# Performance work log

Measured on AMD Instinct MI355X. Metric: run time of the kernel, lower is better.

## Reference

```python
import math
import jax, jax.numpy as jnp
import numpy as np

B, S, D, H = 2, 2048, 1024, 16
DH = D // H
EPS = 1e-5


def setup_inputs() -> dict:
    key = jax.random.key(0)
    ks = jax.random.split(key, 8)
    def lin(k, din, dout):
        return jax.random.normal(k, (din, dout), dtype=jnp.float32) / math.sqrt(din)
    return {
        "x": jax.random.normal(ks[0], (B, S, D), dtype=jnp.float32),
        "attention_mask": jnp.ones((B, S), dtype=jnp.int32),
        "Wq": lin(ks[1], D, D),
        "Wk": lin(ks[2], D, D),
        "Wv": lin(ks[3], D, D),
        "Wo": lin(ks[4], D, D),
        "W1": lin(ks[5], D, 4 * D),
        "W2": lin(ks[6], 2 * D, D),
        "gamma1": jnp.ones((D,), jnp.float32),
        "beta1": jnp.zeros((D,), jnp.float32),
        "gamma2": jnp.ones((D,), jnp.float32),
        "beta2": jnp.zeros((D,), jnp.float32),
    }


def layernorm(x, gamma, beta):
    mu = jnp.mean(x, axis=-1, keepdims=True)
    xc = x - mu
    var = jnp.mean(xc * xc, axis=-1, keepdims=True)
    return gamma * (xc / jnp.sqrt(var + EPS)) + beta


def softmax_last(x):
    x = x - jnp.max(x, axis=-1, keepdims=True)
    e = jnp.exp(x)
    return e / jnp.sum(e, axis=-1, keepdims=True)


def mhsa(x, attention_mask, Wq, Wk, Wv, Wo, causal=True):
    b, s, d = x.shape
    q = (x @ Wq).reshape(b, s, H, DH).transpose(0, 2, 1, 3)  # [b,h,s,dh]
    k = (x @ Wk).reshape(b, s, H, DH).transpose(0, 2, 1, 3)
    v = (x @ Wv).reshape(b, s, H, DH).transpose(0, 2, 1, 3)
    score = jnp.einsum("bhqd,bhkd->bhqk", q, k) / math.sqrt(DH)
    if causal:
        cmask = jnp.tril(jnp.ones((s, s), dtype=bool))
        score = jnp.where(cmask[None, None], score, -jnp.inf)
    key_mask = attention_mask.astype(bool)[:, None, None, :]  # [b,1,1,s]
    score = jnp.where(key_mask, score, -jnp.inf)
    attn = softmax_last(score)
    out = jnp.einsum("bhqk,bhkd->bhqd", attn, v)
    out = out.transpose(0, 2, 1, 3).reshape(b, s, d)
    return out @ Wo


def reference(x, attention_mask, Wq, Wk, Wv, Wo, W1, W2, gamma1, beta1, gamma2, beta2):
    x1 = x + mhsa(layernorm(x, gamma1, beta1), attention_mask, Wq, Wk, Wv, Wo, causal=True)
    h = layernorm(x1, gamma2, beta2) @ W1          # [b,s,4d]
    left, right = h[:, :, : 2 * D], h[:, :, 2 * D :]
    glu = left * jax.nn.sigmoid(right)             # [b,s,2d]
    return x1 + glu @ W2
```

## Files before the change

kernel.cpp:

```cpp
#include <hip/hip_runtime.h>
#include <hip/hip_bf16.h>
#include <math.h>

#define BB 2
#define SS 2048
#define DD 1024
#define HH 16
#define DH 64
#define NTOK (BB * SS)
#define LN_EPS 1e-5f
#define BIGNEG -1e30f

typedef __attribute__((ext_vector_type(8))) short bf16x8;
typedef __attribute__((ext_vector_type(4))) float f32x4;

static __device__ __forceinline__ unsigned short f2bu(float f) {
    __hip_bfloat16 h = __float2bfloat16(f);
    return *(unsigned short*)&h;
}

static __device__ __forceinline__ void async16(const void* g, void* l) {
    __builtin_amdgcn_global_load_lds((const __attribute__((address_space(1))) void*)g,
                                     (__attribute__((address_space(3))) void*)l, 16, 0, 0);
}


__global__ __launch_bounds__(256) void prep_kernel(const float* __restrict__ Wq,
                                                   const float* __restrict__ Wk,
                                                   const float* __restrict__ Wv,
                                                   const float* __restrict__ Wo,
                                                   const float* __restrict__ W1,
                                                   const float* __restrict__ W2,
                                                   __hip_bfloat16* __restrict__ wqkvt,
                                                   __hip_bfloat16* __restrict__ wot,
                                                   __hip_bfloat16* __restrict__ w1t,
                                                   __hip_bfloat16* __restrict__ w2t,
                                                   const float* __restrict__ x,
                                                   const float* __restrict__ gamma,
                                                   const float* __restrict__ beta,
                                                   __hip_bfloat16* __restrict__ lnb) {
    __shared__ float t[32][33];
    __shared__ float red[256];
    const int bid = blockIdx.x;
    const int tid = threadIdx.x;

    if (bid >= 10240) {
        const int row = bid - 10240;
        const float* xp = x + (size_t)row * DD;
        float vals[4];
        float s = 0.f;
#pragma unroll
        for (int i = 0; i < 4; ++i) {
            float v = xp[tid + i * 256];
            vals[i] = v;
            s += v;
        }
        red[tid] = s;
        __syncthreads();
        for (int st = 128; st > 0; st >>= 1) {
            if (tid < st) red[tid] += red[tid + st];
            __syncthreads();
        }
        const float mu = red[0] * (1.0f / DD);
        __syncthreads();
        float sq = 0.f;
#pragma unroll
        for (int i = 0; i < 4; ++i) {
            float d = vals[i] - mu;
            sq += d * d;
        }
        red[tid] = sq;
        __syncthreads();
        for (int st = 128; st > 0; st >>= 1) {
            if (tid < st) red[tid] += red[tid + st];
            __syncthreads();
        }
        const float rinv = rsqrtf(red[0] * (1.0f / DD) + LN_EPS);
        __hip_bfloat16* op = lnb + (size_t)row * DD;
#pragma unroll
        for (int i = 0; i < 4; ++i) {
            int j = tid + i * 256;
            op[j] = __float2bfloat16(gamma[j] * ((vals[i] - mu) * rinv) + beta[j]);
        }
        return;
    }

    const float* W;
    __hip_bfloat16* Wt;
    int K, N, tile;
    if (bid < 4096) {
        const int m = bid >> 10;
        tile = bid & 1023;
        W = (m == 0) ? Wq : (m == 1) ? Wk : (m == 2) ? Wv : Wo;
        Wt = (m < 3) ? (wqkvt + (size_t)m * 1024 * 1024) : wot;
        K = 1024; N = 1024;
    } else if (bid < 8192) {
        tile = bid - 4096; W = W1; Wt = w1t; K = 1024; N = 4096;
    } else {
        tile = bid - 8192; W = W2; Wt = w2t; K = 2048; N = 1024;
    }
    const int nt = N >> 5;
    const int n0 = (tile % nt) * 32, k0 = (tile / nt) * 32;
    const int tx = tid & 31, ty = tid >> 5;
#pragma unroll
    for (int i = 0; i < 4; ++i)
        t[ty + 8 * i][tx] = W[(size_t)(k0 + ty + 8 * i) * N + n0 + tx];
    __syncthreads();
#pragma unroll
    for (int i = 0; i < 4; ++i)
        Wt[(size_t)(n0 + ty + 8 * i) * K + k0 + tx] = __float2bfloat16(t[tx][ty + 8 * i]);
}

__global__ __launch_bounds__(256) void ln_kernel(const float* __restrict__ x,
                                                 const float* __restrict__ gamma,
                                                 const float* __restrict__ beta,
                                                 __hip_bfloat16* __restrict__ out) {
    const int row = blockIdx.x;
    const int tid = threadIdx.x;
    __shared__ float red[256];

    const float* xp = x + (size_t)row * DD;
    float vals[4];
    float s = 0.f;
#pragma unroll
    for (int i = 0; i < 4; ++i) {
        float v = xp[tid + i * 256];
        vals[i] = v;
        s += v;
    }
    red[tid] = s;
    __syncthreads();
    for (int st = 128; st > 0; st >>= 1) {
        if (tid < st) red[tid] += red[tid + st];
        __syncthreads();
    }
    const float mu = red[0] * (1.0f / DD);
    __syncthreads();
    float sq = 0.f;
#pragma unroll
    for (int i = 0; i < 4; ++i) {
        float d = vals[i] - mu;
        sq += d * d;
    }
    red[tid] = sq;
    __syncthreads();
    for (int st = 128; st > 0; st >>= 1) {
        if (tid < st) red[tid] += red[tid + st];
        __syncthreads();
    }
    const float rinv = rsqrtf(red[0] * (1.0f / DD) + LN_EPS);

    __hip_bfloat16* op = out + (size_t)row * DD;
#pragma unroll
    for (int i = 0; i < 4; ++i) {
        int j = tid + i * 256;
        op[j] = __float2bfloat16(gamma[j] * ((vals[i] - mu) * rinv) + beta[j]);
    }
}

__global__ __launch_bounds__(256) void vtrans(const __hip_bfloat16* __restrict__ qkvb_,
                                              __hip_bfloat16* __restrict__ VT_) {
    const unsigned short* src = (const unsigned short*)qkvb_;
    unsigned short* dst = (unsigned short*)VT_;
    __shared__ unsigned short t[64][65];
    const int c0 = (blockIdx.x & 15) << 6;
    const int t0 = (blockIdx.x >> 4) << 6;
    const int tx = threadIdx.x & 63, ty = threadIdx.x >> 6;
#pragma unroll
    for (int i = 0; i < 16; ++i)
        t[ty + 4 * i][tx] = src[(size_t)(t0 + ty + 4 * i) * 3072 + 2048 + c0 + tx];
    __syncthreads();
#pragma unroll
    for (int i = 0; i < 16; ++i)
        dst[(size_t)(c0 + ty + 4 * i) * 4096 + t0 + tx] = t[tx][ty + 4 * i];
}

template <int RES, int EPI>
__global__ __launch_bounds__(256) void mfma_gemm(const __hip_bfloat16* __restrict__ A,
                                                 const __hip_bfloat16* __restrict__ Bt,
                                                 const void* __restrict__ res,
                                                 void* __restrict__ out,
                                                 int M, int N, int K) {
    __shared__ short As[128 * 64];
    __shared__ short Bs[128 * 64];
    const int tid = threadIdx.x;
    const int lane = tid & 63;
    const int wave = tid >> 6;
    const int row0 = blockIdx.y * 128;
    const int col0 = blockIdx.x * 128;
    const int wr = (wave >> 1) * 64;
    const int wc = (wave & 1) * 64;
    const int l15 = lane & 15;
    const int quad = lane >> 4;
    const int s7 = l15 & 7;

    f32x4 acc[4][4] = {};

    for (int k0 = 0; k0 < K; k0 += 64) {
#pragma unroll
        for (int r = 0; r < 4; ++r) {
            const int ec = r * 256 + tid;
            const int ar = ec >> 3, d = ec & 7;
            const int ao = (d ^ (ar & 7)) << 3;
            async16(&A[(size_t)(row0 + ar) * K + k0 + ao], &As[ec << 3]);
            async16(&Bt[(size_t)(col0 + ar) * K + k0 + ao], &Bs[ec << 3]);
        }
        __syncthreads();
#pragma unroll
        for (int kk = 0; kk < 2; ++kk) {
            const int co = (((kk << 2) | quad) ^ s7) << 3;
            bf16x8 af[4], bfr[4];
#pragma unroll
            for (int i = 0; i < 4; ++i)
                af[i] = *(const bf16x8*)&As[(wr + i * 16 + l15) * 64 + co];
#pragma unroll
            for (int j = 0; j < 4; ++j)
                bfr[j] = *(const bf16x8*)&Bs[(wc + j * 16 + l15) * 64 + co];
#pragma unroll
            for (int i = 0; i < 4; ++i)
#pragma unroll
                for (int j = 0; j < 4; ++j)
                    acc[i][j] = __builtin_amdgcn_mfma_f32_16x16x32_bf16(af[i], bfr[j], acc[i][j], 0, 0, 0);
        }
        __syncthreads();
    }

    const int r4 = quad * 4;
#pragma unroll
    for (int i = 0; i < 4; ++i) {
#pragma unroll
        for (int j = 0; j < 4; ++j) {
            const int orow0 = row0 + wr + i * 16 + r4;
            const int ocol = col0 + wc + j * 16 + l15;
#pragma unroll
            for (int rg = 0; rg < 4; ++rg) {
                const size_t oi = (size_t)(orow0 + rg) * N + ocol;
                float v = acc[i][j][rg];
                if constexpr (RES == 1) v += ((const float*)res)[oi];
                if constexpr (EPI == 0) ((float*)out)[oi] = v;
                if constexpr (EPI == 1) ((__hip_bfloat16*)out)[oi] = __float2bfloat16(v);
            }
        }
    }
}

template <int RES, int EPI>
__global__ __launch_bounds__(256) void mfma_gemm_n64(const __hip_bfloat16* __restrict__ A,
                                                     const __hip_bfloat16* __restrict__ Bt,
                                                     const void* __restrict__ res,
                                                     void* __restrict__ out,
                                                     int N, int K, int colTiles) {
    __shared__ short As[128 * 64];
    __shared__ short Bs[64 * 64];
    const int tid = threadIdx.x;
    const int lane = tid & 63;
    const int wave = tid >> 6;
    const int cpx = gridDim.x >> 3;
    const int wg = (blockIdx.x & 7) * cpx + (blockIdx.x >> 3);
    const int row0 = (wg / colTiles) * 128;
    const int col0 = (wg % colTiles) * 64;
    const int wr = wave * 32;
    const int l15 = lane & 15;
    const int quad = lane >> 4;
    const int s7 = l15 & 7;

    f32x4 acc[2][4] = {};

    for (int k0 = 0; k0 < K; k0 += 64) {
#pragma unroll
        for (int r = 0; r < 4; ++r) {
            const int ec = r * 256 + tid;
            const int ar = ec >> 3, d = ec & 7;
            const int ao = (d ^ (ar & 7)) << 3;
            async16(&A[(size_t)(row0 + ar) * K + k0 + ao], &As[ec << 3]);
        }
#pragma unroll
        for (int r = 0; r < 2; ++r) {
            const int ec = r * 256 + tid;
            const int ar = ec >> 3, d = ec & 7;
            const int ao = (d ^ (ar & 7)) << 3;
            async16(&Bt[(size_t)(col0 + ar) * K + k0 + ao], &Bs[ec << 3]);
        }
        __syncthreads();
#pragma unroll
        for (int kk = 0; kk < 2; ++kk) {
            const int co = (((kk << 2) | quad) ^ s7) << 3;
            bf16x8 af[2], bfr[4];
#pragma unroll
            for (int i = 0; i < 2; ++i)
                af[i] = *(const bf16x8*)&As[(wr + i * 16 + l15) * 64 + co];
#pragma unroll
            for (int j = 0; j < 4; ++j)
                bfr[j] = *(const bf16x8*)&Bs[(j * 16 + l15) * 64 + co];
#pragma unroll
            for (int i = 0; i < 2; ++i)
#pragma unroll
                for (int j = 0; j < 4; ++j)
                    acc[i][j] = __builtin_amdgcn_mfma_f32_16x16x32_bf16(af[i], bfr[j], acc[i][j], 0, 0, 0);
        }
        __syncthreads();
    }

    const int r4 = quad * 4;
#pragma unroll
    for (int i = 0; i < 2; ++i) {
#pragma unroll
        for (int j = 0; j < 4; ++j) {
            const int orow0 = row0 + wr + i * 16 + r4;
            const int ocol = col0 + j * 16 + l15;
#pragma unroll
            for (int rg = 0; rg < 4; ++rg) {
                const size_t oi = (size_t)(orow0 + rg) * N + ocol;
                float v = acc[i][j][rg];
                if constexpr (RES == 1) v += ((const float*)res)[oi];
                if constexpr (EPI == 0) ((float*)out)[oi] = v;
                if constexpr (EPI == 1) ((__hip_bfloat16*)out)[oi] = __float2bfloat16(v);
            }
        }
    }
}

__global__ __launch_bounds__(256) void mfma_gemm_glu64(const __hip_bfloat16* __restrict__ A,
                                                       const __hip_bfloat16* __restrict__ Bt,
                                                       __hip_bfloat16* __restrict__ out) {
    __shared__ short As[128 * 64];
    __shared__ short Bl[64 * 64];
    __shared__ short Br[64 * 64];
    const int tid = threadIdx.x;
    const int lane = tid & 63;
    const int wave = tid >> 6;
    const int cpx = gridDim.x >> 3;
    const int wg = (blockIdx.x & 7) * cpx + (blockIdx.x >> 3);
    const int row0 = (wg >> 5) * 128;
    const int col0 = (wg & 31) * 64;
    const int wr = wave * 32;
    const int l15 = lane & 15;
    const int quad = lane >> 4;
    const int s7 = l15 & 7;

    f32x4 accl[2][4] = {};
    f32x4 accr[2][4] = {};

    for (int k0 = 0; k0 < 1024; k0 += 64) {
#pragma unroll
        for (int r = 0; r < 4; ++r) {
            const int ec = r * 256 + tid;
            const int ar = ec >> 3, d = ec & 7;
            const int ao = (d ^ (ar & 7)) << 3;
            async16(&A[(size_t)(row0 + ar) * 1024 + k0 + ao], &As[ec << 3]);
        }
#pragma unroll
        for (int r = 0; r < 2; ++r) {
            const int ec = r * 256 + tid;
            const int ar = ec >> 3, d = ec & 7;
            const int ao = (d ^ (ar & 7)) << 3;
            async16(&Bt[(size_t)(col0 + ar) * 1024 + k0 + ao], &Bl[ec << 3]);
            async16(&Bt[(size_t)(2048 + col0 + ar) * 1024 + k0 + ao], &Br[ec << 3]);
        }
        __syncthreads();
#pragma unroll
        for (int kk = 0; kk < 2; ++kk) {
            const int co = (((kk << 2) | quad) ^ s7) << 3;
            bf16x8 af[2], bl[4], br[4];
#pragma unroll
            for (int i = 0; i < 2; ++i)
                af[i] = *(const bf16x8*)&As[(wr + i * 16 + l15) * 64 + co];
#pragma unroll
            for (int j = 0; j < 4; ++j) {
                bl[j] = *(const bf16x8*)&Bl[(j * 16 + l15) * 64 + co];
                br[j] = *(const bf16x8*)&Br[(j * 16 + l15) * 64 + co];
            }
#pragma unroll
            for (int i = 0; i < 2; ++i)
#pragma unroll
                for (int j = 0; j < 4; ++j) {
                    accl[i][j] = __builtin_amdgcn_mfma_f32_16x16x32_bf16(af[i], bl[j], accl[i][j], 0, 0, 0);
                    accr[i][j] = __builtin_amdgcn_mfma_f32_16x16x32_bf16(af[i], br[j], accr[i][j], 0, 0, 0);
                }
        }
        __syncthreads();
    }

    const int r4 = quad * 4;
#pragma unroll
    for (int i = 0; i < 2; ++i) {
#pragma unroll
        for (int j = 0; j < 4; ++j) {
#pragma unroll
            for (int rg = 0; rg < 4; ++rg) {
                const int orow = row0 + wr + i * 16 + r4 + rg;
                const int ocol = col0 + j * 16 + l15;
                const float l = accl[i][j][rg];
                const float r = accr[i][j][rg];
                out[(size_t)orow * 2048 + ocol] =
                    __float2bfloat16(l * (1.f / (1.f + __expf(-r))));
            }
        }
    }
}

#define KADV (64 * 3072)
#define RESCALE_THR 8.f
__global__ __launch_bounds__(256, 4) void flash_mfma(const __hip_bfloat16* __restrict__ qkv_,
                                                     const __hip_bfloat16* __restrict__ VT_,
                                                     const int* __restrict__ mask,
                                                     __hip_bfloat16* __restrict__ attnb) {
    const unsigned short* qkv = (const unsigned short*)qkv_;
    const unsigned short* VT = (const unsigned short*)VT_;
    __shared__ __align__(16) short Ks[2][64 * 64];
    __shared__ __align__(16) short Vt[2][64 * 64];
    __shared__ __align__(16) short Ps[4][16 * 64];

    const int tid = threadIdx.x;
    const int lane = tid & 63;
    const int wave = tid >> 6;
    const int l15 = lane & 15;
    const int quad = lane >> 4;
    const int s7 = l15 & 7;

    const int xcd = blockIdx.x & 7;
    const int slot = blockIdx.x >> 3;
    const int bh = xcd + ((slot & 3) << 3);
    const int v = slot >> 2;
    const int vr = v & 7, vs = v >> 3;
    const int qt = (vs == 0) ? 31 - vr : (vs == 1) ? vr : (vs == 2) ? 23 - vr : 8 + vr;
    const int h = bh & 15;
    const int b = bh >> 4;
    const int q0 = qt * 64 + wave * 16;

    const int e0 = tid, e1 = 256 + tid;
    const int r0 = e0 >> 3, d0 = e0 & 7, r1 = e1 >> 3, d1 = e1 & 7;
    const unsigned short* kp0 = qkv + (size_t)(b * SS + r0) * 3072 + 1024 + h * 64 + ((d0 ^ (r0 & 7)) << 3);
    const unsigned short* kp1 = qkv + (size_t)(b * SS + r1) * 3072 + 1024 + h * 64 + ((d1 ^ (r1 & 7)) << 3);
    const unsigned short* vp0 = VT + (size_t)(h * 64 + r0) * 4096 + b * SS + ((d0 ^ (r0 & 7)) << 3);
    const unsigned short* vp1 = VT + (size_t)(h * 64 + r1) * 4096 + b * SS + ((d1 ^ (r1 & 7)) << 3);
    short* const kd0a = &Ks[0][e0 << 3]; short* const kd0b = &Ks[1][e0 << 3];
    short* const kd1a = &Ks[0][e1 << 3]; short* const kd1b = &Ks[1][e1 << 3];
    short* const vd0a = &Vt[0][e0 << 3]; short* const vd0b = &Vt[1][e0 << 3];
    short* const vd1a = &Vt[0][e1 << 3]; short* const vd1b = &Vt[1][e1 << 3];

    const int* const mrow = mask + b * SS;

    bf16x8 aq[2];
#pragma unroll
    for (int ks = 0; ks < 2; ++ks)
        aq[ks] = *(const bf16x8*)(qkv + (size_t)(b * SS + q0 + l15) * 3072 +
                                  h * 64 + ks * 32 + quad * 8);

    f32x4 O[4];
#pragma unroll
    for (int i = 0; i < 4; ++i) O[i] = (f32x4){0.f, 0.f, 0.f, 0.f};
    float m_r = BIGNEG, l_r = 0.f;

    const int nch = qt + 1;

    async16(kp0, kd0a); async16(kp1, kd1a);
    async16(vp0, vd0a); async16(vp1, vd1a);
    kp0 += KADV; kp1 += KADV; vp0 += 64; vp1 += 64;

    for (int c = 0; c < nch; ++c) {
        const int cur = c & 1;
        __syncthreads();

        if (c + 1 < nch) {
            async16(kp0, cur ? kd0a : kd0b);
            async16(kp1, cur ? kd1a : kd1b);
            async16(vp0, cur ? vd0a : vd0b);
            async16(vp1, cur ? vd1a : vd1b);
            kp0 += KADV; kp1 += KADV; vp0 += 64; vp1 += 64;
        }

        const int kb = c << 6;
        const int dq = q0 - kb;
        if (dq + 15 < 0) continue;

        int ktmax = ((dq + 15) >> 4) + 1;
        if (ktmax > 4) ktmax = 4;
        int ktfull = (dq - 15) >= 0 ? ((dq - 15) >> 4) + 1 : 0;
        if (ktfull > 4) ktfull = 4;
        const short* Kc = &Ks[cur][0];
        const short* Vc = &Vt[cur][0];

        int4 mv[4];
#pragma unroll
        for (int kt = 0; kt < 4; ++kt) {
            if (kt >= ktmax) break;
            mv[kt] = *(const int4*)&mrow[kb + kt * 16 + quad * 4];
        }

        f32x4 S[4];
        __builtin_amdgcn_s_setprio(1);
#pragma unroll
        for (int kt = 0; kt < 4; ++kt) {
            if (kt >= ktmax) break;
            const bf16x8 bk0 = *(const bf16x8*)&Kc[(kt * 16 + l15) * 64 + ((quad ^ s7) << 3)];
            const bf16x8 bk1 = *(const bf16x8*)&Kc[(kt * 16 + l15) * 64 + (((4 | quad) ^ s7) << 3)];
            f32x4 z = {0.f, 0.f, 0.f, 0.f};
            z = __builtin_amdgcn_mfma_f32_16x16x32_bf16(bk0, aq[0], z, 0, 0, 0);
            S[kt] = __builtin_amdgcn_mfma_f32_16x16x32_bf16(bk1, aq[1], z, 0, 0, 0);
        }
        __builtin_amdgcn_s_setprio(0);

        const int qrow = q0 + l15;
#pragma unroll
        for (int kt = 0; kt < 4; ++kt) {
            if (kt >= ktmax) break;
            const int* mm = (const int*)&mv[kt];
#pragma unroll
            for (int rg = 0; rg < 4; ++rg) {
                float s = fmaf(S[kt][rg], 0.125f, mm[rg] ? 0.f : BIGNEG);
                if (kt >= ktfull) {
                    const int key = kb + kt * 16 + quad * 4 + rg;
                    s = (key <= qrow) ? s : BIGNEG;
                }
                S[kt][rg] = s;
            }
        }

        float tmax = BIGNEG;
#pragma unroll
        for (int kt = 0; kt < 4; ++kt) {
            if (kt >= ktmax) break;
            tmax = fmaxf(tmax, fmaxf(fmaxf(S[kt][0], S[kt][1]),
                                     fmaxf(S[kt][2], S[kt][3])));
        }
        tmax = fmaxf(tmax, __shfl_xor(tmax, 16));
        tmax = fmaxf(tmax, __shfl_xor(tmax, 32));

        if (__any(tmax > m_r + RESCALE_THR)) {
            const float mn = fmaxf(m_r, tmax);
            const float alpha = __expf(m_r - mn);
            m_r = mn;
            l_r *= alpha;
#pragma unroll
            for (int nt = 0; nt < 4; ++nt)
#pragma unroll
                for (int rg = 0; rg < 4; ++rg)
                    O[nt][rg] *= alpha;
        }

        float rsum = 0.f;
#pragma unroll
        for (int kt = 0; kt < 4; ++kt) {
            if (kt >= ktmax) break;
#pragma unroll
            for (int rg = 0; rg < 4; ++rg)
                S[kt][rg] = __expf(S[kt][rg] - m_r);
            rsum += (S[kt][0] + S[kt][1]) + (S[kt][2] + S[kt][3]);
        }
        rsum += __shfl_xor(rsum, 16);
        rsum += __shfl_xor(rsum, 32);
        l_r += rsum;

        short* Pw = &Ps[wave][0];
        asm volatile("s_waitcnt lgkmcnt(0)" ::: "memory");
#pragma unroll
        for (int kt = 0; kt < 4; ++kt) {
            if (kt >= ktmax) break;
            const int ch = (kt << 1) | (quad >> 1);
            const int base = (l15 << 6) + (((ch ^ s7) << 3) | ((quad & 1) << 2));
            const unsigned p0 = ((unsigned)f2bu(S[kt][1]) << 16) | f2bu(S[kt][0]);
            const unsigned p1 = ((unsigned)f2bu(S[kt][3]) << 16) | f2bu(S[kt][2]);
            *(unsigned*)&Pw[base] = p0;
            *(unsigned*)&Pw[base + 2] = p1;
        }
        const int kkmax = (ktmax + 1) >> 1;
        if (ktmax & 1) {
            const int ch = (ktmax << 1) | (quad >> 1);
            const int base = (l15 << 6) + (((ch ^ s7) << 3) | ((quad & 1) << 2));
            *(unsigned*)&Pw[base] = 0;
            *(unsigned*)&Pw[base + 2] = 0;
        }
        asm volatile("s_waitcnt lgkmcnt(0)" ::: "memory");
        __builtin_amdgcn_s_setprio(1);
#pragma unroll
        for (int kk = 0; kk < 2; ++kk) {
            if (kk >= kkmax) break;
            const bf16x8 bp = *(const bf16x8*)&Pw[(l15 << 6) + ((((kk << 2) | quad) ^ s7) << 3)];
#pragma unroll
            for (int nt = 0; nt < 4; ++nt) {
                const bf16x8 av = *(const bf16x8*)&Vc[(nt * 16 + l15) * 64 +
                                                     ((((kk << 2) | quad) ^ s7) << 3)];
                O[nt] = __builtin_amdgcn_mfma_f32_16x16x32_bf16(av, bp, O[nt], 0, 0, 0);
            }
        }
        __builtin_amdgcn_s_setprio(0);
    }

    const float inv = 1.f / l_r;
    unsigned short* op = (unsigned short*)attnb +
                         (size_t)(b * SS + q0 + l15) * 1024 + h * 64 + quad * 4;
#pragma unroll
    for (int nt = 0; nt < 4; ++nt) {
        const float o0 = O[nt][0] * inv, o1 = O[nt][1] * inv;
        const float o2 = O[nt][2] * inv, o3 = O[nt][3] * inv;
        const unsigned long long pk =
            (unsigned long long)(((unsigned)f2bu(o3) << 16) | f2bu(o2)) << 32 |
            (((unsigned)f2bu(o1) << 16) | f2bu(o0));
        *(unsigned long long*)(op + nt * 16) = pk;
    }
}

extern "C" void kernel_launch(void* const* d_in, const int* in_sizes, int n_in,
                              void* d_out, int out_size, void* d_ws, size_t ws_size,
                              hipStream_t stream) {
    const float* x  = (const float*)d_in[0];
    const int* mask = (const int*)d_in[1];
    const float* Wq = (const float*)d_in[2];
    const float* Wk = (const float*)d_in[3];
    const float* Wv = (const float*)d_in[4];
    const float* Wo = (const float*)d_in[5];
    const float* W1 = (const float*)d_in[6];
    const float* W2 = (const float*)d_in[7];
    const float* g1 = (const float*)d_in[8];
    const float* b1 = (const float*)d_in[9];
    const float* g2 = (const float*)d_in[10];
    const float* b2 = (const float*)d_in[11];

    const size_t MB = 1024 * 1024;
    uint8_t* ws = (uint8_t*)d_ws;
    __hip_bfloat16* wqkvt = (__hip_bfloat16*)(ws);
    __hip_bfloat16* wot   = (__hip_bfloat16*)(ws + 6 * MB);
    __hip_bfloat16* w1t   = (__hip_bfloat16*)(ws + 8 * MB);
    __hip_bfloat16* w2t   = (__hip_bfloat16*)(ws + 16 * MB);
    __hip_bfloat16* lnb   = (__hip_bfloat16*)(ws + 20 * MB);
    __hip_bfloat16* qkvb  = (__hip_bfloat16*)(ws + 28 * MB);
    float*          x1    = (float*)(ws + 28 * MB);
    __hip_bfloat16* attnb = (__hip_bfloat16*)(ws + 52 * MB);
    __hip_bfloat16* VT    = (__hip_bfloat16*)(ws + 60 * MB);
    __hip_bfloat16* glub  = (__hip_bfloat16*)(ws + 68 * MB);

    prep_kernel<<<10240 + NTOK, 256, 0, stream>>>(Wq, Wk, Wv, Wo, W1, W2,
                                                  wqkvt, wot, w1t, w2t,
                                                  x, g1, b1, lnb);

    mfma_gemm<0, 1><<<dim3(24, 32), 256, 0, stream>>>(lnb, wqkvt, nullptr, qkvb, NTOK, 3072, 1024);

    vtrans<<<1024, 256, 0, stream>>>(qkvb, VT);

    flash_mfma<<<1024, 256, 0, stream>>>(qkvb, VT, mask, attnb);

    mfma_gemm_n64<1, 0><<<512, 256, 0, stream>>>(attnb, wot, x, x1, 1024, 1024, 16);

    ln_kernel<<<NTOK, 256, 0, stream>>>(x1, g2, b2, lnb);

    mfma_gemm_glu64<<<1024, 256, 0, stream>>>(lnb, w1t, glub);

    mfma_gemm_n64<1, 0><<<512, 256, 0, stream>>>(glub, w2t, x1, (float*)d_out,
                                                 1024, 2048, 16);
}
```

Measured before the change: 209.9 us.

## Pass P tile through registers via permlane16_swap instead of LDS round-trip

The bf16 P fragment is no longer staged through per-wave shared memory. It is packed in registers and rearranged across lanes with permlane16_swap to form the MFMA B operand. To match the new lane-to-k mapping, the V read offset is permuted to the same order. This removes LDS writes and reads plus two lgkmcnt waits. It also frees shared memory, so launch bounds rise to 5 blocks per CU, at the cost of tighter register limits and a dependence on lane-permutation correctness.

```diff
diff --git a/kernel.cpp b/kernel.cpp
--- a/kernel.cpp
+++ b/kernel.cpp
@@ -401,7 +401,9 @@
 
 #define KADV (64 * 3072)
 #define RESCALE_THR 8.f
-__global__ __launch_bounds__(256, 4) void flash_mfma(const __hip_bfloat16* __restrict__ qkv_,
+typedef __attribute__((ext_vector_type(2))) unsigned int uint2v;
+
+__global__ __launch_bounds__(256, 5) void flash_mfma(const __hip_bfloat16* __restrict__ qkv_,
                                                      const __hip_bfloat16* __restrict__ VT_,
                                                      const int* __restrict__ mask,
                                                      __hip_bfloat16* __restrict__ attnb) {
@@ -409,7 +411,6 @@
     const unsigned short* VT = (const unsigned short*)VT_;
     __shared__ __align__(16) short Ks[2][64 * 64];
     __shared__ __align__(16) short Vt[2][64 * 64];
-    __shared__ __align__(16) short Ps[4][16 * 64];
 
     const int tid = threadIdx.x;
     const int lane = tid & 63;
@@ -417,6 +418,7 @@
     const int l15 = lane & 15;
     const int quad = lane >> 4;
     const int s7 = l15 & 7;
+    const int cq = ((quad & 1) << 1) | (quad >> 1);
 
     const int xcd = blockIdx.x & 7;
     const int slot = blockIdx.x >> 3;
@@ -539,6 +541,9 @@
                     O[nt][rg] *= alpha;
         }
 
+        unsigned p[4][2];
+#pragma unroll
+        for (int kt = 0; kt < 4; ++kt) { p[kt][0] = 0u; p[kt][1] = 0u; }
         float rsum = 0.f;
 #pragma unroll
         for (int kt = 0; kt < 4; ++kt) {
@@ -547,40 +552,30 @@
             for (int rg = 0; rg < 4; ++rg)
                 S[kt][rg] = __expf(S[kt][rg] - m_r);
             rsum += (S[kt][0] + S[kt][1]) + (S[kt][2] + S[kt][3]);
+            p[kt][0] = ((unsigned)f2bu(S[kt][1]) << 16) | f2bu(S[kt][0]);
+            p[kt][1] = ((unsigned)f2bu(S[kt][3]) << 16) | f2bu(S[kt][2]);
         }
         rsum += __shfl_xor(rsum, 16);
         rsum += __shfl_xor(rsum, 32);
         l_r += rsum;
 
-        short* Pw = &Ps[wave][0];
-        asm volatile("s_waitcnt lgkmcnt(0)" ::: "memory");
-#pragma unroll
-        for (int kt = 0; kt < 4; ++kt) {
-            if (kt >= ktmax) break;
-            const int ch = (kt << 1) | (quad >> 1);
-            const int base = (l15 << 6) + (((ch ^ s7) << 3) | ((quad & 1) << 2));
-            const unsigned p0 = ((unsigned)f2bu(S[kt][1]) << 16) | f2bu(S[kt][0]);
-            const unsigned p1 = ((unsigned)f2bu(S[kt][3]) << 16) | f2bu(S[kt][2]);
-            *(unsigned*)&Pw[base] = p0;
-            *(unsigned*)&Pw[base + 2] = p1;
-        }
         const int kkmax = (ktmax + 1) >> 1;
-        if (ktmax & 1) {
-            const int ch = (ktmax << 1) | (quad >> 1);
-            const int base = (l15 << 6) + (((ch ^ s7) << 3) | ((quad & 1) << 2));
-            *(unsigned*)&Pw[base] = 0;
-            *(unsigned*)&Pw[base + 2] = 0;
-        }
-        asm volatile("s_waitcnt lgkmcnt(0)" ::: "memory");
         __builtin_amdgcn_s_setprio(1);
 #pragma unroll
         for (int kk = 0; kk < 2; ++kk) {
             if (kk >= kkmax) break;
-            const bf16x8 bp = *(const bf16x8*)&Pw[(l15 << 6) + ((((kk << 2) | quad) ^ s7) << 3)];
+            const uint2v w0 = __builtin_amdgcn_permlane16_swap(p[kk * 2][0], p[kk * 2 + 1][0], false, false);
+            const uint2v w1 = __builtin_amdgcn_permlane16_swap(p[kk * 2][1], p[kk * 2 + 1][1], false, false);
+            union { unsigned u[4]; bf16x8 v; } bpu;
+            bpu.u[0] = w0[0];
+            bpu.u[1] = w1[0];
+            bpu.u[2] = w0[1];
+            bpu.u[3] = w1[1];
+            const bf16x8 bp = bpu.v;
+            const int co = (((cq + (kk << 2))) ^ s7) << 3;
 #pragma unroll
             for (int nt = 0; nt < 4; ++nt) {
-                const bf16x8 av = *(const bf16x8*)&Vc[(nt * 16 + l15) * 64 +
-                                                     ((((kk << 2) | quad) ^ s7) << 3)];
+                const bf16x8 av = *(const bf16x8*)&Vc[(nt * 16 + l15) * 64 + co];
                 O[nt] = __builtin_amdgcn_mfma_f32_16x16x32_bf16(av, bp, O[nt], 0, 0, 0);
             }
         }
```

Measured after the change: 218.0 us. +3.9%, slower.
